# Optimization experiments

Measured on AMD Instinct MI355X. Metric: run time of the kernel, lower is better.

## Reference

```python
import jax, jax.numpy as jnp
import numpy as np

THRESHOLDS = (0.25, 0.375, 0.5, 0.625)
NUM_CLASSES = 5
SMOOTH = 1e-5  # dice smoothing constant


def setup_inputs() -> dict:
    key = jax.random.key(0)
    k1, k2 = jax.random.split(key)
    # [N, T, C, H, W]; input has 5 class channels, target 1 intensity channel
    inp = jax.random.uniform(k1, (4, 10, 5, 384, 384), dtype=jnp.float32)
    tgt = jax.random.uniform(k2, (4, 10, 1, 384, 384), dtype=jnp.float32)
    weight = jnp.array([1.0, 1.0, 2.0, 5.0, 10.0], dtype=jnp.float32)
    return {"input": inp, "target": tgt, "weight": weight}


def reference(input, target, weight):
    # permute to [N, C, T, H, W]
    x = jnp.transpose(input, (0, 2, 1, 3, 4))   # [N,5,T,H,W]
    t = jnp.transpose(target, (0, 2, 1, 3, 4))  # [N,1,T,H,W]
    # threshold binning: class index = number of thresholds <= target value
    cls = jnp.zeros(t.shape, dtype=jnp.int32)
    for thr in THRESHOLDS:
        cls = cls + (t >= thr).astype(jnp.int32)
    # one-hot scatter along class dim -> [N,5,T,H,W]
    class_ids = jnp.arange(NUM_CLASSES, dtype=jnp.int32).reshape(1, NUM_CLASSES, 1, 1, 1)
    onehot = (cls == class_ids).astype(x.dtype)
    # per-class dice over all remaining dims
    axes = (0, 2, 3, 4)
    inter = jnp.sum(x * onehot, axis=axes)                      # [5]
    denom = jnp.sum(x, axis=axes) + jnp.sum(onehot, axis=axes)  # [5]
    dice_loss = 1.0 - (2.0 * inter + SMOOTH) / (denom + SMOOTH)  # [5]
    return jnp.sum(weight * dice_loss)
```

## Files before the change

### kernel.cpp

```cpp
#include <hip/hip_runtime.h>

#define HW      147456
#define NC      5
#define NT      40
#define GPS     36864
#define BX      72
#define TPS     (BX * 256)
#define NBLK    (BX * NT)
#define SMOOTH  1e-5f


__global__ __launch_bounds__(256) void dice_main(const float* __restrict__ inp,
                                                 const float* __restrict__ tgt,
                                                 float* __restrict__ ws) {
    const int nt = blockIdx.y;
    const int t0 = blockIdx.x * 256 + threadIdx.x;

    const float* __restrict__ tb = tgt + (size_t)nt * (size_t)HW;
    const float* __restrict__ ib = inp + (size_t)nt * (size_t)(NC * HW);

    float sumx[NC]  = {0.f, 0.f, 0.f, 0.f, 0.f};
    float inter[NC] = {0.f, 0.f, 0.f, 0.f, 0.f};
    float cnt[NC]   = {0.f, 0.f, 0.f, 0.f, 0.f};

    #pragma unroll
    for (int it = 0; it < 2; ++it) {
        const int g = t0 + it * TPS;
        const float4 t4 = reinterpret_cast<const float4*>(tb)[g];

        const int c0 = (t4.x >= 0.25f) + (t4.x >= 0.375f) + (t4.x >= 0.5f) + (t4.x >= 0.625f);
        const int c1 = (t4.y >= 0.25f) + (t4.y >= 0.375f) + (t4.y >= 0.5f) + (t4.y >= 0.625f);
        const int c2 = (t4.z >= 0.25f) + (t4.z >= 0.375f) + (t4.z >= 0.5f) + (t4.z >= 0.625f);
        const int c3 = (t4.w >= 0.25f) + (t4.w >= 0.375f) + (t4.w >= 0.5f) + (t4.w >= 0.625f);

        const float* base = ib + ((size_t)g << 2);
        #pragma unroll
        for (int c = 0; c < NC; ++c) {
            const float4 x4 = *reinterpret_cast<const float4*>(base + (size_t)c * HW);
            sumx[c] += (x4.x + x4.y) + (x4.z + x4.w);
            float iv = 0.f;
            if (c0 == c) iv += x4.x;
            if (c1 == c) iv += x4.y;
            if (c2 == c) iv += x4.z;
            if (c3 == c) iv += x4.w;
            inter[c] += iv;
            cnt[c]   += (float)((c0 == c) + (c1 == c) + (c2 == c) + (c3 == c));
        }
    }

    float v[15];
    #pragma unroll
    for (int c = 0; c < NC; ++c) { v[c] = sumx[c]; v[5 + c] = inter[c]; v[10 + c] = cnt[c]; }

    #pragma unroll
    for (int j = 0; j < 15; ++j) {
        #pragma unroll
        for (int off = 32; off > 0; off >>= 1)
            v[j] += __shfl_down(v[j], off, 64);
    }

    __shared__ float part[4][15];
    const int lane = threadIdx.x & 63;
    const int wv   = threadIdx.x >> 6;
    if (lane == 0) {
        #pragma unroll
        for (int j = 0; j < 15; ++j) part[wv][j] = v[j];
    }
    __syncthreads();
    if (threadIdx.x < 15) {
        const float s = part[0][threadIdx.x] + part[1][threadIdx.x] +
                        part[2][threadIdx.x] + part[3][threadIdx.x];
        ws[threadIdx.x * NBLK + (blockIdx.y * BX + blockIdx.x)] = s;
    }
}

__global__ __launch_bounds__(960) void dice_final(const float* __restrict__ ws,
                                                  const float* __restrict__ w,
                                                  float* __restrict__ out) {
    __shared__ float red[15];
    const int j    = threadIdx.x >> 6;
    const int lane = threadIdx.x & 63;

    float s = 0.f;
    for (int b = lane; b < NBLK; b += 64)
        s += ws[j * NBLK + b];

    #pragma unroll
    for (int off = 32; off > 0; off >>= 1)
        s += __shfl_down(s, off, 64);

    if (lane == 0) red[j] = s;
    __syncthreads();

    if (threadIdx.x == 0) {
        float loss = 0.f;
        #pragma unroll
        for (int c = 0; c < NC; ++c) {
            const float inter = red[5 + c];
            const float denom = red[c] + red[10 + c];
            loss += w[c] * (1.f - (2.f * inter + SMOOTH) / (denom + SMOOTH));
        }
        out[0] = loss;
    }
}

extern "C" void kernel_launch(void* const* d_in, const int* in_sizes, int n_in,
                              void* d_out, int out_size, void* d_ws, size_t ws_size,
                              hipStream_t stream) {
    const float* inp = (const float*)d_in[0];
    const float* tgt = (const float*)d_in[1];
    const float* wgt = (const float*)d_in[2];
    float* out = (float*)d_out;
    float* ws  = (float*)d_ws;

    dice_main<<<dim3(BX, NT), 256, 0, stream>>>(inp, tgt, ws);
    dice_final<<<1, 960, 0, stream>>>(ws, wgt, out);
}
```

Before: 202.5 us.

## Split dice reduction across class channels with per-class blocks and batched loads

Each block now handles a single class channel (grid gains a class dimension), so each thread accumulates only 3 values instead of 15. It issues all of its loads up front, four float4 loads each of target and input. This cuts register pressure and the shuffle reductions, and keeps more loads in flight. In exchange, the target tensor is read five times, once per class, which adds memory traffic to a bandwidth-bound kernel, though L2 or the MALL may absorb some of it.

Measured after the change: 191.3 us. -5.5%, faster.

```diff
diff --git a/kernel.cpp b/kernel.cpp
--- a/kernel.cpp
+++ b/kernel.cpp
@@ -1,76 +1,76 @@
 #include <hip/hip_runtime.h>
 
 #define HW      147456
+#define GPS     36864
 #define NC      5
 #define NT      40
-#define GPS     36864
-#define BX      72
-#define TPS     (BX * 256)
-#define NBLK    (BX * NT)
+#define BX      36
+#define ITERS   4
+#define NPB     1440
 #define SMOOTH  1e-5f
 
 
 __global__ __launch_bounds__(256) void dice_main(const float* __restrict__ inp,
                                                  const float* __restrict__ tgt,
                                                  float* __restrict__ ws) {
-    const int nt = blockIdx.y;
-    const int t0 = blockIdx.x * 256 + threadIdx.x;
+    const int c  = blockIdx.y;
+    const int nt = blockIdx.z;
+    const int g0 = blockIdx.x * 1024 + threadIdx.x;
 
-    const float* __restrict__ tb = tgt + (size_t)nt * (size_t)HW;
-    const float* __restrict__ ib = inp + (size_t)nt * (size_t)(NC * HW);
+    const float4* __restrict__ tb =
+        reinterpret_cast<const float4*>(tgt + (size_t)nt * (size_t)HW);
+    const float4* __restrict__ ib =
+        reinterpret_cast<const float4*>(inp + ((size_t)nt * NC + c) * (size_t)HW);
 
-    float sumx[NC]  = {0.f, 0.f, 0.f, 0.f, 0.f};
-    float inter[NC] = {0.f, 0.f, 0.f, 0.f, 0.f};
-    float cnt[NC]   = {0.f, 0.f, 0.f, 0.f, 0.f};
-
+    float4 t4[ITERS], x4[ITERS];
     #pragma unroll
-    for (int it = 0; it < 2; ++it) {
-        const int g = t0 + it * TPS;
-        const float4 t4 = reinterpret_cast<const float4*>(tb)[g];
-
-        const int c0 = (t4.x >= 0.25f) + (t4.x >= 0.375f) + (t4.x >= 0.5f) + (t4.x >= 0.625f);
-        const int c1 = (t4.y >= 0.25f) + (t4.y >= 0.375f) + (t4.y >= 0.5f) + (t4.y >= 0.625f);
-        const int c2 = (t4.z >= 0.25f) + (t4.z >= 0.375f) + (t4.z >= 0.5f) + (t4.z >= 0.625f);
-        const int c3 = (t4.w >= 0.25f) + (t4.w >= 0.375f) + (t4.w >= 0.5f) + (t4.w >= 0.625f);
-
-        const float* base = ib + ((size_t)g << 2);
-        #pragma unroll
-        for (int c = 0; c < NC; ++c) {
-            const float4 x4 = *reinterpret_cast<const float4*>(base + (size_t)c * HW);
-            sumx[c] += (x4.x + x4.y) + (x4.z + x4.w);
-            float iv = 0.f;
-            if (c0 == c) iv += x4.x;
-            if (c1 == c) iv += x4.y;
-            if (c2 == c) iv += x4.z;
-            if (c3 == c) iv += x4.w;
-            inter[c] += iv;
-            cnt[c]   += (float)((c0 == c) + (c1 == c) + (c2 == c) + (c3 == c));
-        }
+    for (int it = 0; it < ITERS; ++it) {
+        const int g = g0 + it * 256;
+        t4[it] = tb[g];
+        x4[it] = ib[g];
     }
 
-    float v[15];
+    float sumx = 0.f, inter = 0.f, cntf = 0.f;
     #pragma unroll
-    for (int c = 0; c < NC; ++c) { v[c] = sumx[c]; v[5 + c] = inter[c]; v[10 + c] = cnt[c]; }
+    for (int it = 0; it < ITERS; ++it) {
+        const float4 t = t4[it];
+        const float4 x = x4[it];
+        sumx += (x.x + x.y) + (x.z + x.w);
 
+        const int b0 = (t.x >= 0.25f) + (t.x >= 0.375f) + (t.x >= 0.5f) + (t.x >= 0.625f);
+        const int b1 = (t.y >= 0.25f) + (t.y >= 0.375f) + (t.y >= 0.5f) + (t.y >= 0.625f);
+        const int b2 = (t.z >= 0.25f) + (t.z >= 0.375f) + (t.z >= 0.5f) + (t.z >= 0.625f);
+        const int b3 = (t.w >= 0.25f) + (t.w >= 0.375f) + (t.w >= 0.5f) + (t.w >= 0.625f);
+
+        float iv = 0.f, cv = 0.f;
+        if (b0 == c) { iv += x.x; cv += 1.f; }
+        if (b1 == c) { iv += x.y; cv += 1.f; }
+        if (b2 == c) { iv += x.z; cv += 1.f; }
+        if (b3 == c) { iv += x.w; cv += 1.f; }
+        inter += iv;
+        cntf  += cv;
+    }
+
+    float v[3] = {sumx, inter, cntf};
     #pragma unroll
-    for (int j = 0; j < 15; ++j) {
+    for (int j = 0; j < 3; ++j) {
         #pragma unroll
         for (int off = 32; off > 0; off >>= 1)
             v[j] += __shfl_down(v[j], off, 64);
     }
 
-    __shared__ float part[4][15];
+    __shared__ float part[4][3];
     const int lane = threadIdx.x & 63;
     const int wv   = threadIdx.x >> 6;
     if (lane == 0) {
         #pragma unroll
-        for (int j = 0; j < 15; ++j) part[wv][j] = v[j];
+        for (int j = 0; j < 3; ++j) part[wv][j] = v[j];
     }
     __syncthreads();
-    if (threadIdx.x < 15) {
+    if (threadIdx.x < 3) {
         const float s = part[0][threadIdx.x] + part[1][threadIdx.x] +
                         part[2][threadIdx.x] + part[3][threadIdx.x];
-        ws[threadIdx.x * NBLK + (blockIdx.y * BX + blockIdx.x)] = s;
+        ws[((size_t)c * 3 + threadIdx.x) * NPB + (nt * BX + blockIdx.x)] = s;
     }
 }
 
@@ -78,26 +78,28 @@
                                                   const float* __restrict__ w,
                                                   float* __restrict__ out) {
     __shared__ float red[15];
-    const int j    = threadIdx.x >> 6;
+    const int s    = threadIdx.x >> 6;
     const int lane = threadIdx.x & 63;
 
-    float s = 0.f;
-    for (int b = lane; b < NBLK; b += 64)
-        s += ws[j * NBLK + b];
+    float acc = 0.f;
+    for (int b = lane; b < NPB; b += 64)
+        acc += ws[s * NPB + b];
 
     #pragma unroll
     for (int off = 32; off > 0; off >>= 1)
-        s += __shfl_down(s, off, 64);
+        acc += __shfl_down(acc, off, 64);
 
-    if (lane == 0) red[j] = s;
+    if (lane == 0) red[s] = acc;
     __syncthreads();
 
     if (threadIdx.x == 0) {
         float loss = 0.f;
         #pragma unroll
         for (int c = 0; c < NC; ++c) {
-            const float inter = red[5 + c];
-            const float denom = red[c] + red[10 + c];
+            const float sumx  = red[c * 3 + 0];
+            const float inter = red[c * 3 + 1];
+            const float cnt   = red[c * 3 + 2];
+            const float denom = sumx + cnt;
             loss += w[c] * (1.f - (2.f * inter + SMOOTH) / (denom + SMOOTH));
         }
         out[0] = loss;
@@ -113,6 +115,6 @@
     float* out = (float*)d_out;
     float* ws  = (float*)d_ws;
 
-    dice_main<<<dim3(BX, NT), 256, 0, stream>>>(inp, tgt, ws);
+    dice_main<<<dim3(BX, NC, NT), 256, 0, stream>>>(inp, tgt, ws);
     dice_final<<<1, 960, 0, stream>>>(ws, wgt, out);
 }
```
